# Kernel tuning notes

Hardware: AMD Instinct MI355X
Metric: run time of the kernel (lower is better)

The kernel has to match this reference:

```python
import jax, jax.numpy as jnp
import numpy as np

D_MODEL = 2048
N_HEADS = 16
KV_HEADS = 4
HEAD_DIM = D_MODEL // N_HEADS  # 128
B, T = 2, 2048


def setup_inputs() -> dict:
    key = jax.random.key(0)
    ks = jax.random.split(key, 8)
    s = 1.0 / np.sqrt(D_MODEL)
    x = jax.random.normal(ks[0], (B, T, D_MODEL), dtype=jnp.float32)
    # Linear weights stored as (in_features, out_features); y = x @ W
    Wq = jax.random.normal(ks[1], (D_MODEL, D_MODEL), dtype=jnp.float32) * s
    Wk = jax.random.normal(ks[2], (D_MODEL, KV_HEADS * HEAD_DIM), dtype=jnp.float32) * s
    Wv = jax.random.normal(ks[3], (D_MODEL, KV_HEADS * HEAD_DIM), dtype=jnp.float32) * s
    Wo = jax.random.normal(ks[4], (D_MODEL, D_MODEL), dtype=jnp.float32) * s
    weight_logits = jnp.ones((KV_HEADS,), dtype=jnp.float32)
    weight_values = jnp.ones((KV_HEADS,), dtype=jnp.float32)
    # additive causal mask (1, 1, T, T): 0 on/below diag, -inf above
    neg_inf = jnp.float32(-1e30)
    causal = jnp.tril(jnp.ones((T, T), dtype=bool))
    attn_mask = jnp.where(causal, jnp.float32(0.0), neg_inf)[None, None]
    return {"x": x, "attn_mask": attn_mask, "Wq": Wq, "Wk": Wk, "Wv": Wv,
            "Wo": Wo, "weight_logits": weight_logits, "weight_values": weight_values}


def reference(x, attn_mask, Wq, Wk, Wv, Wo, weight_logits, weight_values):
    Bx, Tx, _ = x.shape
    H, G, D = N_HEADS, KV_HEADS, HEAD_DIM
    group_size = H // G
    head_to_group = jnp.arange(H) // group_size  # (H,)

    q = (x @ Wq).reshape(Bx, Tx, H, D).transpose(0, 2, 1, 3)  # (B,H,T,D)
    k = (x @ Wk).reshape(Bx, Tx, G, D).transpose(0, 2, 1, 3)  # (B,G,T,D)
    v = (x @ Wv).reshape(Bx, Tx, G, D).transpose(0, 2, 1, 3)  # (B,G,T,D)

    # GQA expansion: gather kv groups per head
    k_g = k[:, head_to_group]  # (B,H,T,D)
    v_g = v[:, head_to_group]  # (B,H,T,D)
    # (use_value_weight=False: weight_values unused)

    logit_scale = weight_logits[head_to_group][None, :, None, None]  # (1,H,1,1)
    inv_sqrt_d = jnp.float32(1.0 / np.sqrt(D))
    logits = jnp.einsum('bhqd,bhkd->bhqk', q, k_g) * inv_sqrt_d * logit_scale
    logits = logits + attn_mask
    attn = jax.nn.softmax(logits, axis=-1)  # dropout p=0 -> identity
    y = jnp.einsum('bhqk,bhkd->bhqd', attn, v_g)
    y = y.transpose(0, 2, 1, 3).reshape(Bx, Tx, H * D)
    return y @ Wo
```

## Files before the change

kernel.cpp:

```cpp
#include <hip/hip_runtime.h>
#include <hip/hip_bf16.h>

#define TT 2048
#define DM 2048
#define NH 16
#define KVH 4
#define HD 128

typedef __attribute__((ext_vector_type(8))) short bs8;
typedef __attribute__((ext_vector_type(4))) float fx4;
typedef __attribute__((ext_vector_type(4))) unsigned short us4;
typedef __attribute__((ext_vector_type(8))) unsigned short us8;

__device__ inline unsigned short f2b(float f) {
  __hip_bfloat16 h = __float2bfloat16(f);
  return *reinterpret_cast<unsigned short*>(&h);
}

__device__ inline float b2f(unsigned short u) {
  unsigned int v = ((unsigned int)u) << 16;
  return *reinterpret_cast<float*>(&v);
}

__device__ inline void gld_lds16(const ushort* g, ushort* l) {
  __builtin_amdgcn_global_load_lds(
      (const __attribute__((address_space(1))) void*)g,
      (__attribute__((address_space(3))) void*)l,
      16, 0, 0);
}

__global__ __launch_bounds__(256) void prep_kernel(
    const float* __restrict__ x, const float* __restrict__ Wq,
    const float* __restrict__ Wk, const float* __restrict__ Wv,
    const float* __restrict__ Wo, ushort* __restrict__ xb,
    ushort* __restrict__ Wqkvt, ushort* __restrict__ Wot) {
  int tx = threadIdx.x, ty = threadIdx.y;
  if (blockIdx.z == 2) {
    int lin = (blockIdx.y * 96 + blockIdx.x) * 256 + ty * 32 + tx;
#pragma unroll
    for (int it = 0; it < 2; ++it) {
      int i = lin + it * (6144 * 256);
      if (i < (TT * 2 * DM) / 4) {
        float4 v = ((const float4*)x)[i];
        us4 o = {f2b(v.x), f2b(v.y), f2b(v.z), f2b(v.w)};
        ((us4*)xb)[i] = o;
      }
    }
    return;
  }
  __shared__ float t[32][33];
  int n0 = blockIdx.x * 32, k0 = blockIdx.y * 32;
  if (blockIdx.z == 0) {
    const float* src;
    int srcN, col0;
    if (n0 < 2048) { src = Wq; srcN = 2048; col0 = n0; }
    else if (n0 < 2560) { src = Wk; srcN = 512; col0 = n0 - 2048; }
    else { src = Wv; srcN = 512; col0 = n0 - 2560; }
    for (int jj = 0; jj < 4; ++jj)
      t[ty + jj * 8][tx] = src[(size_t)(k0 + ty + jj * 8) * srcN + col0 + tx];
    __syncthreads();
    for (int jj = 0; jj < 4; ++jj)
      Wqkvt[(size_t)(n0 + ty + jj * 8) * 2048 + k0 + tx] = f2b(t[tx][ty + jj * 8]);
  } else {
    if (n0 >= 2048) return;
    for (int jj = 0; jj < 4; ++jj)
      t[ty + jj * 8][tx] = Wo[(size_t)(k0 + ty + jj * 8) * 2048 + n0 + tx];
    __syncthreads();
    for (int jj = 0; jj < 4; ++jj)
      Wot[(size_t)(n0 + ty + jj * 8) * 2048 + k0 + tx] = f2b(t[tx][ty + jj * 8]);
  }
}

#define EPI_STRIDE 136
__global__ __launch_bounds__(256) void gemm_qkv(const ushort* __restrict__ A,
                                                const ushort* __restrict__ Bt,
                                                ushort* __restrict__ qo,
                                                ushort* __restrict__ ko,
                                                ushort* __restrict__ vo,
                                                int K) {
  __shared__ alignas(16) ushort smem[128 * EPI_STRIDE];
  ushort* As = smem;
  ushort* Bs = smem + 8192;
  const int tid = threadIdx.x;
  const int lane = tid & 63;
  const int wid = tid >> 6;
  const int wm = wid >> 1, wn = wid & 1;
  const int quad = lane >> 4, l16 = lane & 15;
  const int bm = blockIdx.y * 128, bn = blockIdx.x * 128;

  fx4 acc[4][4];
  for (int i = 0; i < 4; ++i)
    for (int j = 0; j < 4; ++j) acc[i][j] = (fx4){0.f, 0.f, 0.f, 0.f};

  const int r8 = lane >> 3, s8 = lane & 7;
  for (int k0 = 0; k0 < K; k0 += 64) {
    for (int i = 0; i < 4; ++i) {
      int m = i * 32 + wid * 8 + r8;
      int c = s8 ^ (m & 7);
      gld_lds16(A + (size_t)(bm + m) * K + k0 + c * 8, As + (i * 32 + wid * 8) * 64);
      gld_lds16(Bt + (size_t)(bn + m) * K + k0 + c * 8, Bs + (i * 32 + wid * 8) * 64);
    }
    __syncthreads();
    for (int ks = 0; ks < 2; ++ks) {
      bs8 af[4], bf[4];
      for (int mt = 0; mt < 4; ++mt) {
        int m = wm * 64 + mt * 16 + l16;
        int c = ks * 4 + quad;
        int slot = c ^ (m & 7);
        af[mt] = *(const bs8*)(As + m * 64 + slot * 8);
      }
      for (int nt = 0; nt < 4; ++nt) {
        int n = wn * 64 + nt * 16 + l16;
        int c = ks * 4 + quad;
        int slot = c ^ (n & 7);
        bf[nt] = *(const bs8*)(Bs + n * 64 + slot * 8);
      }
      for (int mt = 0; mt < 4; ++mt)
        for (int nt = 0; nt < 4; ++nt)
          acc[mt][nt] = __builtin_amdgcn_mfma_f32_16x16x32_bf16(af[mt], bf[nt],
                                                                acc[mt][nt], 0, 0, 0);
    }
    __syncthreads();
  }

  for (int mt = 0; mt < 4; ++mt)
    for (int nt = 0; nt < 4; ++nt)
      for (int r = 0; r < 4; ++r) {
        int row = wm * 64 + mt * 16 + quad * 4 + r;
        int col = wn * 64 + nt * 16 + l16;
        smem[row * EPI_STRIDE + col] = f2b(acc[mt][nt][r]);
      }
  __syncthreads();
  const int rsel = tid >> 4;
  const int csel = tid & 15;
  for (int ii = 0; ii < 8; ++ii) {
    int row = ii * 16 + rsel;
    us8 chunk = *(const us8*)(smem + row * EPI_STRIDE + csel * 8);
    int row_g = bm + row;
    int colc = bn + csel * 8;
    if (bn < 2048) {
      *(us8*)(qo + (size_t)row_g * 2048 + colc) = chunk;
    } else {
      int b = row_g >> 11, t = row_g & 2047;
      if (bn < 2560) {
        int kc = colc - 2048;
        int gg = kc >> 7, d = kc & 127;
        *(us8*)(ko + ((size_t)(b * KVH + gg) * TT + t) * HD + d) = chunk;
      } else {
        int vc = colc - 2560;
        int gg = vc >> 7, d = vc & 127;
        *(us8*)(vo + ((size_t)(b * KVH + gg) * TT + t) * HD + d) = chunk;
      }
    }
  }
}

__global__ __launch_bounds__(256) void transpose_v(const ushort* __restrict__ vin,
                                                   ushort* __restrict__ vout) {
  __shared__ ushort tl[32][33];
  int tx = threadIdx.x, ty = threadIdx.y;
  int t0 = blockIdx.x * 32, d0 = blockIdx.y * 32;
  size_t base = (size_t)blockIdx.z * TT * HD;
  for (int jj = 0; jj < 4; ++jj)
    tl[ty + jj * 8][tx] = vin[base + (size_t)(t0 + ty + jj * 8) * HD + d0 + tx];
  __syncthreads();
  for (int jj = 0; jj < 4; ++jj)
    vout[base + (size_t)(d0 + ty + jj * 8) * TT + t0 + tx] = tl[tx][ty + jj * 8];
}

__global__ __launch_bounds__(256) void gemm_out(const ushort* __restrict__ A,
                                                const ushort* __restrict__ Bt,
                                                float* __restrict__ Cout,
                                                int N, int K) {
  __shared__ alignas(16) ushort smem[128 * EPI_STRIDE];
  ushort* As = smem;
  ushort* Bs = smem + 8192;
  const int tid = threadIdx.x;
  const int lane = tid & 63;
  const int wid = tid >> 6;
  const int wm = wid >> 1, wn = wid & 1;
  const int quad = lane >> 4, l16 = lane & 15;
  const int bm = blockIdx.y * 128, bn = blockIdx.x * 128;

  fx4 acc[4][4];
  for (int i = 0; i < 4; ++i)
    for (int j = 0; j < 4; ++j) acc[i][j] = (fx4){0.f, 0.f, 0.f, 0.f};

  const int r8 = lane >> 3, s8 = lane & 7;
  for (int k0 = 0; k0 < K; k0 += 64) {
    for (int i = 0; i < 4; ++i) {
      int m = i * 32 + wid * 8 + r8;
      int c = s8 ^ (m & 7);
      gld_lds16(A + (size_t)(bm + m) * K + k0 + c * 8, As + (i * 32 + wid * 8) * 64);
      gld_lds16(Bt + (size_t)(bn + m) * K + k0 + c * 8, Bs + (i * 32 + wid * 8) * 64);
    }
    __syncthreads();
    for (int ks = 0; ks < 2; ++ks) {
      bs8 af[4], bf[4];
      for (int mt = 0; mt < 4; ++mt) {
        int m = wm * 64 + mt * 16 + l16;
        int c = ks * 4 + quad;
        int slot = c ^ (m & 7);
        af[mt] = *(const bs8*)(As + m * 64 + slot * 8);
      }
      for (int nt = 0; nt < 4; ++nt) {
        int n = wn * 64 + nt * 16 + l16;
        int c = ks * 4 + quad;
        int slot = c ^ (n & 7);
        bf[nt] = *(const bs8*)(Bs + n * 64 + slot * 8);
      }
      for (int mt = 0; mt < 4; ++mt)
        for (int nt = 0; nt < 4; ++nt)
          acc[mt][nt] = __builtin_amdgcn_mfma_f32_16x16x32_bf16(af[mt], bf[nt],
                                                                acc[mt][nt], 0, 0, 0);
    }
    __syncthreads();
  }

  for (int mt = 0; mt < 4; ++mt)
    for (int nt = 0; nt < 4; ++nt)
      for (int r = 0; r < 4; ++r) {
        int row = wm * 64 + mt * 16 + quad * 4 + r;
        int col = wn * 64 + nt * 16 + l16;
        smem[row * EPI_STRIDE + col] = f2b(acc[mt][nt][r]);
      }
  __syncthreads();
  const int rsel = tid >> 4;
  const int csel = tid & 15;
  for (int ii = 0; ii < 8; ++ii) {
    int row = ii * 16 + rsel;
    us8 chunk = *(const us8*)(smem + row * EPI_STRIDE + csel * 8);
    int row_g = bm + row;
    int colc = bn + csel * 8;
    float4 lo = {b2f(chunk[0]), b2f(chunk[1]), b2f(chunk[2]), b2f(chunk[3])};
    float4 hi = {b2f(chunk[4]), b2f(chunk[5]), b2f(chunk[6]), b2f(chunk[7])};
    *(float4*)(Cout + (size_t)row_g * N + colc) = lo;
    *(float4*)(Cout + (size_t)row_g * N + colc + 4) = hi;
  }
}

__global__ __launch_bounds__(512, 4) void attn_kernel(const ushort* __restrict__ qb,
                                                      const ushort* __restrict__ kb,
                                                      const ushort* __restrict__ vt,
                                                      ushort* __restrict__ yb,
                                                      const float* __restrict__ wlog) {
  __shared__ alignas(16) ushort Ks[64 * 128];
  __shared__ alignas(16) ushort Vs[128 * 64];
  __shared__ alignas(16) ushort Ps[128 * 72];

  const int bid = blockIdx.x;
  const int qt = (bid & 256) ? (bid & 15) : 15 - (bid & 15);
  const int h = (bid >> 4) & 15;
  const int b = bid >> 8;
  const int g = h >> 2;
  const int tid = threadIdx.x;
  const int lane = tid & 63;
  const int wid = tid >> 6;
  const int quad = lane >> 4;
  const int l16 = lane & 15;
  const int qw = qt * 128 + wid * 16;

  const float scale = wlog[g] * 0.08838834764831845f;

  bs8 qf[4];
  {
    int q = qw + l16;
    const ushort* qrow = qb + ((size_t)(b * TT + q)) * DM + h * HD;
#pragma unroll
    for (int ks = 0; ks < 4; ++ks)
      qf[ks] = *(const bs8*)(qrow + ks * 32 + quad * 8);
  }

  float m_i = -INFINITY;
  float l_i = 0.f;
  fx4 o[8];
#pragma unroll
  for (int i = 0; i < 8; ++i) o[i] = (fx4){0.f, 0.f, 0.f, 0.f};

  const ushort* kbase = kb + (size_t)(b * KVH + g) * TT * HD;
  const ushort* vbase = vt + (size_t)(b * KVH + g) * HD * TT;

  const ushort* kp;
  const ushort* vp;
  {
    int keyr = wid * 4 + (lane >> 4);
    int si = lane & 15;
    int ck = (si & 8) | ((si ^ keyr) & 7);
    kp = kbase + (size_t)keyr * HD + ck * 8;
    int dr = wid * 8 + (lane >> 3);
    int s8 = lane & 7;
    int cv = s8 ^ (dr & 7);
    vp = vbase + (size_t)dr * TT + cv * 8;
  }

  const int jmax = 2 * qt + 1;
  for (int j = 0; j <= jmax; ++j) {
    gld_lds16(kp, Ks + wid * 512);
    gld_lds16(kp + 32 * HD, Ks + 4096 + wid * 512);
    gld_lds16(vp, Vs + wid * 512);
    gld_lds16(vp + 64 * TT, Vs + 4096 + wid * 512);
    kp += 64 * HD;
    vp += 64;
    __syncthreads();

    if (j * 64 <= qw + 15) {
      fx4 s[4];
#pragma unroll
      for (int mt = 0; mt < 4; ++mt) s[mt] = (fx4){0.f, 0.f, 0.f, 0.f};
#pragma unroll
      for (int mt = 0; mt < 4; ++mt) {
        bs8 a[4];
        int key = mt * 16 + l16;
#pragma unroll
        for (int ks = 0; ks < 4; ++ks) {
          int c = ks * 4 + quad;
          int slot = (c & 8) | ((c ^ key) & 7);
          a[ks] = *(const bs8*)(Ks + key * 128 + slot * 8);
        }
#pragma unroll
        for (int ks = 0; ks < 4; ++ks)
          s[mt] = __builtin_amdgcn_mfma_f32_16x16x32_bf16(a[ks], qf[ks],
                                                          s[mt], 0, 0, 0);
      }

      const int q = qw + l16;
      if (j * 64 + 63 > qw) {
#pragma unroll
        for (int mt = 0; mt < 4; ++mt)
#pragma unroll
          for (int r = 0; r < 4; ++r) {
            int key = j * 64 + mt * 16 + quad * 4 + r;
            if (key > q) s[mt][r] = -1e30f;
          }
      }
      float mx = s[0][0];
#pragma unroll
      for (int mt = 0; mt < 4; ++mt)
#pragma unroll
        for (int r = 0; r < 4; ++r) mx = fmaxf(mx, s[mt][r]);
      mx = fmaxf(mx, __shfl_xor(mx, 16));
      mx = fmaxf(mx, __shfl_xor(mx, 32));
      float m_new = fmaxf(m_i, mx);
      float alpha = __expf((m_i - m_new) * scale);
      float negb = -m_new * scale;
      float sum = 0.f;
#pragma unroll
      for (int mt = 0; mt < 4; ++mt)
#pragma unroll
        for (int r = 0; r < 4; ++r) {
          float pv = __expf(fmaf(s[mt][r], scale, negb));
          s[mt][r] = pv;
          sum += pv;
        }
      sum += __shfl_xor(sum, 16);
      sum += __shfl_xor(sum, 32);
      l_i = l_i * alpha + sum;
      m_i = m_new;
#pragma unroll
      for (int dmt = 0; dmt < 8; ++dmt)
#pragma unroll
        for (int r = 0; r < 4; ++r) o[dmt][r] *= alpha;

      int qrow = wid * 16 + l16;
#pragma unroll
      for (int mt = 0; mt < 4; ++mt) {
        us4 pw = {f2b(s[mt][0]), f2b(s[mt][1]), f2b(s[mt][2]), f2b(s[mt][3])};
        *(us4*)(Ps + qrow * 72 + mt * 16 + quad * 4) = pw;
      }

#pragma unroll
      for (int ks = 0; ks < 2; ++ks) {
        bs8 pb = *(const bs8*)(Ps + qrow * 72 + ks * 32 + quad * 8);
#pragma unroll
        for (int dmt = 0; dmt < 8; ++dmt) {
          int d = dmt * 16 + l16;
          int c = ks * 4 + quad;
          int slot = c ^ (d & 7);
          bs8 va = *(const bs8*)(Vs + d * 64 + slot * 8);
          o[dmt] = __builtin_amdgcn_mfma_f32_16x16x32_bf16(va, pb, o[dmt], 0, 0, 0);
        }
      }
    }
    __syncthreads();
  }

  {
    float inv = 1.0f / l_i;
    int q = qw + l16;
    ushort* yrow = yb + ((size_t)(b * TT + q)) * DM + h * HD;
#pragma unroll
    for (int dmt = 0; dmt < 8; ++dmt) {
      us4 w = {f2b(o[dmt][0] * inv), f2b(o[dmt][1] * inv),
               f2b(o[dmt][2] * inv), f2b(o[dmt][3] * inv)};
      *(us4*)(yrow + dmt * 16 + quad * 4) = w;
    }
  }
}

extern "C" void kernel_launch(void* const* d_in, const int* in_sizes, int n_in,
                              void* d_out, int out_size, void* d_ws, size_t ws_size,
                              hipStream_t stream) {
  const float* x = (const float*)d_in[0];
  const float* Wq = (const float*)d_in[2];
  const float* Wk = (const float*)d_in[3];
  const float* Wv = (const float*)d_in[4];
  const float* Wo = (const float*)d_in[5];
  const float* wlog = (const float*)d_in[6];

  char* ws = (char*)d_ws;
  ushort* xb = (ushort*)ws;     ws += (size_t)4096 * 2048 * 2;
  ushort* Wqkvt = (ushort*)ws;  ws += (size_t)3072 * 2048 * 2;
  ushort* Wot = (ushort*)ws;    ws += (size_t)2048 * 2048 * 2;
  ushort* qbuf = (ushort*)ws;   ws += (size_t)4096 * 2048 * 2;
  ushort* kbuf = (ushort*)ws;   ws += (size_t)2 * KVH * 2048 * 128 * 2;
  ushort* vtmp = (ushort*)ws;   ws += (size_t)2 * KVH * 2048 * 128 * 2;
  ushort* vbuf = (ushort*)ws;   ws += (size_t)2 * KVH * 2048 * 128 * 2;
  ushort* ybuf = (ushort*)ws;   ws += (size_t)4096 * 2048 * 2;

  prep_kernel<<<dim3(96, 64, 3), dim3(32, 8), 0, stream>>>(
      x, Wq, Wk, Wv, Wo, xb, Wqkvt, Wot);
  gemm_qkv<<<dim3(24, 32), 256, 0, stream>>>(xb, Wqkvt, qbuf, kbuf, vtmp, 2048);
  transpose_v<<<dim3(64, 4, 8), dim3(32, 8), 0, stream>>>(vtmp, vbuf);
  attn_kernel<<<512, 512, 0, stream>>>(qbuf, kbuf, vbuf, ybuf, wlog);
  gemm_out<<<dim3(16, 32), 256, 0, stream>>>(ybuf, Wot, (float*)d_out, 2048, 2048);
}
```

Before: 309.5 us.

## Double-buffer K/V tiles in attention with lazy rescale and exp2 softmax

```diff
diff --git a/kernel.cpp b/kernel.cpp
--- a/kernel.cpp
+++ b/kernel.cpp
@@ -11,6 +11,12 @@
 typedef __attribute__((ext_vector_type(4))) float fx4;
 typedef __attribute__((ext_vector_type(4))) unsigned short us4;
 typedef __attribute__((ext_vector_type(8))) unsigned short us8;
+
+#if __has_builtin(__builtin_amdgcn_exp2f)
+#define EXP2(x) __builtin_amdgcn_exp2f(x)
+#else
+#define EXP2(x) exp2f(x)
+#endif
 
 __device__ inline unsigned short f2b(float f) {
   __hip_bfloat16 h = __float2bfloat16(f);
@@ -244,9 +250,9 @@
                                                       const ushort* __restrict__ vt,
                                                       ushort* __restrict__ yb,
                                                       const float* __restrict__ wlog) {
-  __shared__ alignas(16) ushort Ks[64 * 128];
-  __shared__ alignas(16) ushort Vs[128 * 64];
-  __shared__ alignas(16) ushort Ps[128 * 72];
+  __shared__ alignas(16) ushort Ks[2][64 * 128];
+  __shared__ alignas(16) ushort Vs[2][128 * 64];
+  __shared__ alignas(16) ushort Ps[128 * 64];
 
   const int bid = blockIdx.x;
   const int qt = (bid & 256) ? (bid & 15) : 15 - (bid & 15);
@@ -261,21 +267,7 @@
   const int qw = qt * 128 + wid * 16;
 
   const float scale = wlog[g] * 0.08838834764831845f;
-
-  bs8 qf[4];
-  {
-    int q = qw + l16;
-    const ushort* qrow = qb + ((size_t)(b * TT + q)) * DM + h * HD;
-#pragma unroll
-    for (int ks = 0; ks < 4; ++ks)
-      qf[ks] = *(const bs8*)(qrow + ks * 32 + quad * 8);
-  }
-
-  float m_i = -INFINITY;
-  float l_i = 0.f;
-  fx4 o[8];
-#pragma unroll
-  for (int i = 0; i < 8; ++i) o[i] = (fx4){0.f, 0.f, 0.f, 0.f};
+  const float sc2 = scale * 1.4426950408889634f;
 
   const ushort* kbase = kb + (size_t)(b * KVH + g) * TT * HD;
   const ushort* vbase = vt + (size_t)(b * KVH + g) * HD * TT;
@@ -293,20 +285,52 @@
     vp = vbase + (size_t)dr * TT + cv * 8;
   }
 
+  gld_lds16(kp, &Ks[0][wid * 512]);
+  gld_lds16(kp + 32 * HD, &Ks[0][4096 + wid * 512]);
+  gld_lds16(vp, &Vs[0][wid * 512]);
+  gld_lds16(vp + 64 * TT, &Vs[0][4096 + wid * 512]);
+  kp += 64 * HD;
+  vp += 64;
+
+  bs8 qf[4];
+  {
+    int q = qw + l16;
+    const ushort* qrow = qb + ((size_t)(b * TT + q)) * DM + h * HD;
+#pragma unroll
+    for (int ks = 0; ks < 4; ++ks)
+      qf[ks] = *(const bs8*)(qrow + ks * 32 + quad * 8);
+  }
+
+  float m_i = -INFINITY;
+  float l_i = 0.f;
+  fx4 o[8];
+#pragma unroll
+  for (int i = 0; i < 8; ++i) o[i] = (fx4){0.f, 0.f, 0.f, 0.f};
+
   const int jmax = 2 * qt + 1;
   for (int j = 0; j <= jmax; ++j) {
-    gld_lds16(kp, Ks + wid * 512);
-    gld_lds16(kp + 32 * HD, Ks + 4096 + wid * 512);
-    gld_lds16(vp, Vs + wid * 512);
-    gld_lds16(vp + 64 * TT, Vs + 4096 + wid * 512);
-    kp += 64 * HD;
-    vp += 64;
-    __syncthreads();
+    const int cur = j & 1;
+    if (j < jmax) {
+      const int nxt = cur ^ 1;
+      gld_lds16(kp, &Ks[nxt][wid * 512]);
+      gld_lds16(kp + 32 * HD, &Ks[nxt][4096 + wid * 512]);
+      gld_lds16(vp, &Vs[nxt][wid * 512]);
+      gld_lds16(vp + 64 * TT, &Vs[nxt][4096 + wid * 512]);
+      kp += 64 * HD;
+      vp += 64;
+      asm volatile("s_waitcnt vmcnt(4)" ::: "memory");
+    } else {
+      asm volatile("s_waitcnt vmcnt(0)" ::: "memory");
+    }
+    __builtin_amdgcn_s_barrier();
 
     if (j * 64 <= qw + 15) {
+      const ushort* Kc = Ks[cur];
+      const ushort* Vc = Vs[cur];
       fx4 s[4];
 #pragma unroll
       for (int mt = 0; mt < 4; ++mt) s[mt] = (fx4){0.f, 0.f, 0.f, 0.f};
+      __builtin_amdgcn_s_setprio(1);
 #pragma unroll
       for (int mt = 0; mt < 4; ++mt) {
         bs8 a[4];
@@ -315,13 +339,14 @@
         for (int ks = 0; ks < 4; ++ks) {
           int c = ks * 4 + quad;
           int slot = (c & 8) | ((c ^ key) & 7);
-          a[ks] = *(const bs8*)(Ks + key * 128 + slot * 8);
+          a[ks] = *(const bs8*)(Kc + key * 128 + slot * 8);
         }
 #pragma unroll
         for (int ks = 0; ks < 4; ++ks)
           s[mt] = __builtin_amdgcn_mfma_f32_16x16x32_bf16(a[ks], qf[ks],
                                                           s[mt], 0, 0, 0);
       }
+      __builtin_amdgcn_s_setprio(0);
 
       const int q = qw + l16;
       if (j * 64 + 63 > qw) {
@@ -340,48 +365,57 @@
         for (int r = 0; r < 4; ++r) mx = fmaxf(mx, s[mt][r]);
       mx = fmaxf(mx, __shfl_xor(mx, 16));
       mx = fmaxf(mx, __shfl_xor(mx, 32));
-      float m_new = fmaxf(m_i, mx);
-      float alpha = __expf((m_i - m_new) * scale);
-      float negb = -m_new * scale;
+
+      if (!__all((mx - m_i) * scale <= 8.0f)) {
+        float m_new = fmaxf(m_i, mx);
+        float alpha = EXP2((m_i - m_new) * sc2);
+        l_i *= alpha;
+#pragma unroll
+        for (int dmt = 0; dmt < 8; ++dmt)
+#pragma unroll
+          for (int r = 0; r < 4; ++r) o[dmt][r] *= alpha;
+        m_i = m_new;
+      }
+      float negb = -m_i * sc2;
       float sum = 0.f;
 #pragma unroll
       for (int mt = 0; mt < 4; ++mt)
 #pragma unroll
         for (int r = 0; r < 4; ++r) {
-          float pv = __expf(fmaf(s[mt][r], scale, negb));
+          float pv = EXP2(fmaf(s[mt][r], sc2, negb));
           s[mt][r] = pv;
           sum += pv;
         }
       sum += __shfl_xor(sum, 16);
       sum += __shfl_xor(sum, 32);
-      l_i = l_i * alpha + sum;
-      m_i = m_new;
-#pragma unroll
-      for (int dmt = 0; dmt < 8; ++dmt)
-#pragma unroll
-        for (int r = 0; r < 4; ++r) o[dmt][r] *= alpha;
+      l_i += sum;
 
       int qrow = wid * 16 + l16;
+      int sw = qrow & 7;
 #pragma unroll
       for (int mt = 0; mt < 4; ++mt) {
         us4 pw = {f2b(s[mt][0]), f2b(s[mt][1]), f2b(s[mt][2]), f2b(s[mt][3])};
-        *(us4*)(Ps + qrow * 72 + mt * 16 + quad * 4) = pw;
+        int chunk = mt * 2 + (quad >> 1);
+        *(us4*)(Ps + qrow * 64 + ((chunk ^ sw) << 3) + ((quad & 1) << 2)) = pw;
       }
 
 #pragma unroll
       for (int ks = 0; ks < 2; ++ks) {
-        bs8 pb = *(const bs8*)(Ps + qrow * 72 + ks * 32 + quad * 8);
+        bs8 pb = *(const bs8*)(Ps + qrow * 64 + (((ks * 4 + quad) ^ sw) << 3));
+        __builtin_amdgcn_s_setprio(1);
 #pragma unroll
         for (int dmt = 0; dmt < 8; ++dmt) {
           int d = dmt * 16 + l16;
           int c = ks * 4 + quad;
           int slot = c ^ (d & 7);
-          bs8 va = *(const bs8*)(Vs + d * 64 + slot * 8);
+          bs8 va = *(const bs8*)(Vc + d * 64 + slot * 8);
           o[dmt] = __builtin_amdgcn_mfma_f32_16x16x32_bf16(va, pb, o[dmt], 0, 0, 0);
         }
-      }
-    }
-    __syncthreads();
+        __builtin_amdgcn_s_setprio(0);
+      }
+    }
+    asm volatile("s_waitcnt lgkmcnt(0)" ::: "memory");
+    __builtin_amdgcn_s_barrier();
   }
 
   {
```

New measurement: 301.8 us. 2.5% less time.
